# Kernel tuning notes

Measured on AMD Instinct MI355X. Metric: run time of the kernel, lower is better.

Reference implementation:

```python
import jax, jax.numpy as jnp
import numpy as np

EMBED = 1024
HEADS = 16
HEAD_DIM = EMBED // HEADS
SCALE = HEAD_DIM ** -0.5


def setup_inputs() -> dict:
    key = jax.random.key(0)
    ks = jax.random.split(key, 9)
    B, N = 2, 2048
    std = EMBED ** -0.5
    return {
        "query": jax.random.normal(ks[0], (B, N, EMBED), jnp.float32),
        "key": jax.random.normal(ks[1], (B, N, EMBED), jnp.float32),
        "value": jax.random.normal(ks[2], (B, N, EMBED), jnp.float32),
        # torch nn.Linear weights are [out, in]; y = x @ W.T + b
        "Wq": jax.random.normal(ks[3], (EMBED, EMBED), jnp.float32) * std,
        "bq": jax.random.normal(ks[4], (EMBED,), jnp.float32) * 0.01,
        "Wk": jax.random.normal(ks[5], (EMBED, EMBED), jnp.float32) * std,
        "bk": jax.random.normal(ks[6], (EMBED,), jnp.float32) * 0.01,
        "Wv": jax.random.normal(ks[7], (EMBED, EMBED), jnp.float32) * std,
        "bv": jax.random.normal(ks[8], (EMBED,), jnp.float32) * 0.01,
    }


def reference(query, key, value, Wq, bq, Wk, bk, Wv, bv):
    B, NQ, _ = query.shape
    NK = key.shape[1]
    q = query @ Wq.T + bq  # [B, NQ, E]
    k = key @ Wk.T + bk    # [B, NK, E]
    v = value @ Wv.T + bv  # [B, NK, E]
    # split heads -> [B, H, N, Dh]
    q = q.reshape(B, NQ, HEADS, HEAD_DIM).transpose(0, 2, 1, 3)
    k = k.reshape(B, NK, HEADS, HEAD_DIM).transpose(0, 2, 1, 3)
    v = v.reshape(B, NK, HEADS, HEAD_DIM).transpose(0, 2, 1, 3)
    attn = jnp.einsum("bhqd,bhkd->bhqk", q, k) * SCALE  # [B, H, NQ, NK]
    attn = jax.nn.softmax(attn, axis=-1)
    out = jnp.einsum("bhqk,bhkd->bhqd", attn, v)  # [B, H, NQ, Dh]
    out = out.transpose(0, 2, 1, 3).reshape(B, NQ, EMBED)
    # o_proj is Identity (odim == embed_dim, o_proj=False); dropout is 0 (eval)
    return out
```

## Files before the change

### kernel.cpp

```cpp
#include <hip/hip_runtime.h>

#define EMB 1024
#define NSEQ 2048
#define NBATCH 2
#define NHEAD 16
#define DHEAD 64
#define QSCALE 0.18033688011112042f

typedef float f32x4 __attribute__((ext_vector_type(4)));
typedef short s16x8 __attribute__((ext_vector_type(8)));
typedef short s16x4 __attribute__((ext_vector_type(4)));

typedef __attribute__((address_space(3))) short lds_short;
typedef __attribute__((address_space(1))) const short glb_short;

__device__ __forceinline__ void gl_lds16(const short* g, short* l) {
    __builtin_amdgcn_global_load_lds((glb_short*)g, (lds_short*)l, 16, 0, 0);
}

__device__ __forceinline__ short bf16r(float f) {
    unsigned u = __float_as_uint(f);
    u += 0x7fffu + ((u >> 16) & 1u);
    return (short)(u >> 16);
}

__device__ __forceinline__ unsigned pkbf(float a, float b) {
#if defined(__has_builtin) && __has_builtin(__builtin_amdgcn_cvt_pk_bf16_f32)
    auto r = __builtin_amdgcn_cvt_pk_bf16_f32(a, b);
    unsigned u;
    __builtin_memcpy(&u, &r, 4);
    return u;
#else
    return ((unsigned)bf16r(a) & 0xffffu) | ((unsigned)bf16r(b) << 16);
#endif
}

__device__ __forceinline__ float fexp2(float x) {
#if defined(__has_builtin) && __has_builtin(__builtin_amdgcn_exp2f)
    return __builtin_amdgcn_exp2f(x);
#else
    return exp2f(x);
#endif
}

__global__ __launch_bounds__(256) void cvt6_kernel(
    const float* __restrict__ s0, const float* __restrict__ s1, const float* __restrict__ s2,
    const float* __restrict__ s3, const float* __restrict__ s4, const float* __restrict__ s5,
    short* __restrict__ d0, short* __restrict__ d1, short* __restrict__ d2,
    short* __restrict__ d3, short* __restrict__ d4, short* __restrict__ d5,
    int n0, int n1, int n2, int n3, int n4, int n5)
{
    const int seg = blockIdx.y;
    const float* s = (seg == 0) ? s0 : (seg == 1) ? s1 : (seg == 2) ? s2
                   : (seg == 3) ? s3 : (seg == 4) ? s4 : s5;
    short* d = (seg == 0) ? d0 : (seg == 1) ? d1 : (seg == 2) ? d2
             : (seg == 3) ? d3 : (seg == 4) ? d4 : d5;
    const int n = (seg == 0) ? n0 : (seg == 1) ? n1 : (seg == 2) ? n2
                : (seg == 3) ? n3 : (seg == 4) ? n4 : n5;

    const int i = (blockIdx.x * 256 + threadIdx.x) * 8;
    if (i >= n) return;
    float4 a = *(const float4*)(s + i);
    float4 b = *(const float4*)(s + i + 4);
    uint4 u = { pkbf(a.x, a.y), pkbf(a.z, a.w), pkbf(b.x, b.y), pkbf(b.z, b.w) };
    *(uint4*)(d + i) = u;
}

__global__ __launch_bounds__(256, 3) void proj2_kernel(
    const short* __restrict__ Xq, const short* __restrict__ Xk, const short* __restrict__ Xv,
    const short* __restrict__ Wq, const short* __restrict__ Wk, const short* __restrict__ Wv,
    const float* __restrict__ bq, const float* __restrict__ bk, const float* __restrict__ bv,
    short* __restrict__ Oq, short* __restrict__ Ok, short* __restrict__ Ov)
{
    const int z = blockIdx.z;
    const short* X    = (z == 0) ? Xq : (z == 1) ? Xk : Xv;
    const short* W    = (z == 0) ? Wq : (z == 1) ? Wk : Wv;
    const float* bias = (z == 0) ? bq : (z == 1) ? bk : bv;
    short* Out        = (z == 0) ? Oq : (z == 1) ? Ok : Ov;
    const float osc   = (z == 0) ? QSCALE : 1.0f;

    const int n0 = blockIdx.x * 128;
    const int m0 = blockIdx.y * 128;

    __shared__ __align__(16) short As[128 * 64];
    __shared__ __align__(16) short Bs[128 * 64];

    const int t    = threadIdx.x;
    const int lane = t & 63;
    const int wave = t >> 6;
    const int r    = lane & 15;
    const int quad = lane >> 4;
    const int wm   = (wave >> 1) * 64;
    const int wn   = (wave & 1) * 64;

    const int p0    = wave * 256 + lane;
    const int row0  = p0 >> 3;
    const int lc0   = (p0 & 7) ^ (row0 & 7);
    const short* gA = X + (size_t)(m0 + row0) * EMB + lc0 * 8;
    const short* gB = W + (size_t)(n0 + row0) * EMB + lc0 * 8;
    short* lA = As + p0 * 8;
    short* lB = Bs + p0 * 8;

    f32x4 acc[4][4];
#pragma unroll
    for (int i = 0; i < 4; ++i)
#pragma unroll
        for (int j = 0; j < 4; ++j)
#pragma unroll
            for (int v = 0; v < 4; ++v) acc[i][j][v] = 0.f;

    for (int k0 = 0; k0 < EMB; k0 += 64) {
#pragma unroll
        for (int i = 0; i < 4; ++i) {
            gl_lds16(gA + k0 + (size_t)8 * i * EMB, lA + i * 512);
            gl_lds16(gB + k0 + (size_t)8 * i * EMB, lB + i * 512);
        }
        __syncthreads();

#pragma unroll
        for (int ks = 0; ks < 2; ++ks) {
            const int fc = ((ks * 4 + quad) ^ (r & 7)) * 8;
            s16x8 af[4], bf[4];
#pragma unroll
            for (int i = 0; i < 4; ++i) af[i] = *(const s16x8*)&As[(wm + i * 16 + r) * 64 + fc];
#pragma unroll
            for (int j = 0; j < 4; ++j) bf[j] = *(const s16x8*)&Bs[(wn + j * 16 + r) * 64 + fc];
#pragma unroll
            for (int i = 0; i < 4; ++i)
#pragma unroll
                for (int j = 0; j < 4; ++j)
                    acc[i][j] = __builtin_amdgcn_mfma_f32_16x16x32_bf16(af[i], bf[j], acc[i][j], 0, 0, 0);
        }
        __syncthreads();
    }

    if (z != 2) {
#pragma unroll
        for (int j = 0; j < 4; ++j) {
            const int gn = n0 + wn + j * 16 + r;
            const float bb = bias[gn];
#pragma unroll
            for (int i = 0; i < 4; ++i)
#pragma unroll
                for (int reg = 0; reg < 4; ++reg) {
                    const int gm = m0 + wm + i * 16 + quad * 4 + reg;
                    Out[(size_t)gm * EMB + gn] = bf16r((acc[i][j][reg] + bb) * osc);
                }
        }
    } else {
#pragma unroll
        for (int j = 0; j < 4; ++j) {
            const int gn = n0 + wn + j * 16 + r;
            const float bb = bias[gn];
            const int hh = gn >> 6;
            const int dd = gn & 63;
#pragma unroll
            for (int i = 0; i < 4; ++i) {
                const int gm = m0 + wm + i * 16 + quad * 4;
                const int bi = gm >> 11;
                const int nn = gm & 2047;
                s16x4 pk;
#pragma unroll
                for (int reg = 0; reg < 4; ++reg) pk[reg] = bf16r(acc[i][j][reg] + bb);
                *(s16x4*)(Out + ((size_t)(bi * NHEAD + hh) * DHEAD + dd) * NSEQ + nn) = pk;
            }
        }
    }
}

__global__ __launch_bounds__(256) void proj_kernel(
    const float* __restrict__ Xq, const float* __restrict__ Xk, const float* __restrict__ Xv,
    const float* __restrict__ Wq, const float* __restrict__ Wk, const float* __restrict__ Wv,
    const float* __restrict__ bq, const float* __restrict__ bk, const float* __restrict__ bv,
    short* __restrict__ Oq, short* __restrict__ Ok, short* __restrict__ Ov)
{
    const int z = blockIdx.z;
    const float* X    = (z == 0) ? Xq : (z == 1) ? Xk : Xv;
    const float* W    = (z == 0) ? Wq : (z == 1) ? Wk : Wv;
    const float* bias = (z == 0) ? bq : (z == 1) ? bk : bv;
    short* Out        = (z == 0) ? Oq : (z == 1) ? Ok : Ov;
    const float osc   = (z == 0) ? QSCALE : 1.0f;

    const int n0 = blockIdx.x * 128;
    const int m0 = blockIdx.y * 128;

    __shared__ __align__(16) short As[128][40];
    __shared__ __align__(16) short Bs[128][40];

    const int t    = threadIdx.x;
    const int lane = t & 63;
    const int wave = t >> 6;
    const int r    = lane & 15;
    const int quad = lane >> 4;
    const int wm   = (wave >> 1) * 64;
    const int wn   = (wave & 1) * 64;

    const int srow = t >> 1;
    const int scol = (t & 1) << 4;

    f32x4 acc[4][4];
#pragma unroll
    for (int i = 0; i < 4; ++i)
#pragma unroll
        for (int j = 0; j < 4; ++j)
#pragma unroll
            for (int v = 0; v < 4; ++v) acc[i][j][v] = 0.f;

    for (int k0 = 0; k0 < EMB; k0 += 32) {
        const float4* xp = (const float4*)(X + (size_t)(m0 + srow) * EMB + k0 + scol);
        const float4* wp = (const float4*)(W + (size_t)(n0 + srow) * EMB + k0 + scol);
        float4 x0 = xp[0], x1 = xp[1], x2 = xp[2], x3 = xp[3];
        float4 w0 = wp[0], w1 = wp[1], w2 = wp[2], w3 = wp[3];
        uint4 a0 = { pkbf(x0.x, x0.y), pkbf(x0.z, x0.w), pkbf(x1.x, x1.y), pkbf(x1.z, x1.w) };
        uint4 a1 = { pkbf(x2.x, x2.y), pkbf(x2.z, x2.w), pkbf(x3.x, x3.y), pkbf(x3.z, x3.w) };
        uint4 b0 = { pkbf(w0.x, w0.y), pkbf(w0.z, w0.w), pkbf(w1.x, w1.y), pkbf(w1.z, w1.w) };
        uint4 b1 = { pkbf(w2.x, w2.y), pkbf(w2.z, w2.w), pkbf(w3.x, w3.y), pkbf(w3.z, w3.w) };
        *(uint4*)&As[srow][scol]     = a0;
        *(uint4*)&As[srow][scol + 8] = a1;
        *(uint4*)&Bs[srow][scol]     = b0;
        *(uint4*)&Bs[srow][scol + 8] = b1;
        __syncthreads();

        s16x8 af[4], bf[4];
#pragma unroll
        for (int i = 0; i < 4; ++i) af[i] = *(const s16x8*)&As[wm + i * 16 + r][quad * 8];
#pragma unroll
        for (int j = 0; j < 4; ++j) bf[j] = *(const s16x8*)&Bs[wn + j * 16 + r][quad * 8];
#pragma unroll
        for (int i = 0; i < 4; ++i)
#pragma unroll
            for (int j = 0; j < 4; ++j)
                acc[i][j] = __builtin_amdgcn_mfma_f32_16x16x32_bf16(af[i], bf[j], acc[i][j], 0, 0, 0);
        __syncthreads();
    }

#pragma unroll
    for (int j = 0; j < 4; ++j) {
        const int gn = n0 + wn + j * 16 + r;
        const float bb = bias[gn];
#pragma unroll
        for (int i = 0; i < 4; ++i)
#pragma unroll
            for (int reg = 0; reg < 4; ++reg) {
                const int gm = m0 + wm + i * 16 + quad * 4 + reg;
                Out[(size_t)gm * EMB + gn] = bf16r((acc[i][j][reg] + bb) * osc);
            }
    }
}

__global__ __launch_bounds__(256) void vtrans_kernel(
    const short* __restrict__ Vp, short* __restrict__ VT)
{
    const int n0 = blockIdx.x * 64;
    const int h  = blockIdx.y;
    const int b  = blockIdx.z;
    __shared__ __align__(16) short L[64][72];

    const int t  = threadIdx.x;
    const int rr = t >> 2;
    const int cc = (t & 3) * 16;

    const short* src = Vp + (size_t)(b * NSEQ + n0 + rr) * EMB + h * DHEAD + cc;
    s16x8 a = *(const s16x8*)src;
    s16x8 c = *(const s16x8*)(src + 8);
    *(s16x8*)&L[rr][cc]     = a;
    *(s16x8*)&L[rr][cc + 8] = c;
    __syncthreads();

    const int d  = t >> 2;
    const int c4 = (t & 3) * 16;
    short vals[16];
#pragma unroll
    for (int i = 0; i < 16; ++i) vals[i] = L[c4 + i][d];
    short* dst = VT + ((size_t)(b * NHEAD + h) * DHEAD + d) * NSEQ + n0 + c4;
    *(s16x8*)dst       = *(s16x8*)&vals[0];
    *(s16x8*)(dst + 8) = *(s16x8*)&vals[8];
}

template<bool PARTIAL>
__global__ __launch_bounds__(256, 3) void attn11_kernel(
    const short* __restrict__ Qp, const short* __restrict__ Kp,
    const short* __restrict__ VT, float* __restrict__ Outp,
    float* __restrict__ Lout)
{
    const int ksplit = PARTIAL ? (blockIdx.x & 1) : 0;
    const int qblk   = (PARTIAL ? (blockIdx.x >> 1) : blockIdx.x) * 128;
    const int h      = blockIdx.y;
    const int b      = blockIdx.z;
    const int nt     = PARTIAL ? 8 : 16;
    const int kt0    = PARTIAL ? ksplit * 8 : 0;

    __shared__ __align__(16) char smem[32768];
    short* Ks   = (short*)smem;
    short* Vs   = (short*)smem + 128 * 64;
    float* fbuf = (float*)smem;

    const int t    = threadIdx.x;
    const int lane = t & 63;
    const int w    = t >> 6;
    const int r    = lane & 15;
    const int quad = lane >> 4;
    const int r7   = r & 7;

    const size_t rowbase = (size_t)b * NSEQ;
    const int    colbase = h * DHEAD;
    const size_t bh64    = (size_t)(b * NHEAD + h) * DHEAD;

    s16x8 qf[2][2];
#pragma unroll
    for (int qs = 0; qs < 2; ++qs)
#pragma unroll
        for (int ks = 0; ks < 2; ++ks)
            qf[qs][ks] = *(const s16x8*)(Qp + (rowbase + qblk + w * 32 + qs * 16 + r) * EMB
                                          + colbase + ks * 32 + quad * 8);

    f32x4 accO[2][4];
#pragma unroll
    for (int qs = 0; qs < 2; ++qs)
#pragma unroll
        for (int dt = 0; dt < 4; ++dt)
#pragma unroll
            for (int v = 0; v < 4; ++v) accO[qs][dt][v] = 0.f;
    float lsum[2] = {0.f, 0.f};
    const f32x4 zf = {0.f, 0.f, 0.f, 0.f};

    const int  krow0 = t >> 3;
    const int  kgc   = ((t & 7) ^ (krow0 & 7)) * 8;
    const int  vrow0 = t >> 4;
    const int  vgc   = ((t & 15) ^ (vrow0 & 7)) * 8;
    const short* gK[4];
    const short* gV[4];
    {
        const short* kb0 = Kp + (rowbase + kt0 * 128 + krow0) * EMB + colbase + kgc;
        const short* vb0 = VT + (bh64 + vrow0) * NSEQ + kt0 * 128 + vgc;
#pragma unroll
        for (int i = 0; i < 4; ++i) {
            gK[i] = kb0 + (size_t)i * 32 * EMB;
            gV[i] = vb0 + (size_t)i * 16 * NSEQ;
        }
    }
    short* lK[4];
    short* lV[4];
#pragma unroll
    for (int i = 0; i < 4; ++i) {
        lK[i] = Ks + (i * 256 + t) * 8;
        lV[i] = Vs + (i * 256 + t) * 8;
    }

    const int kofs = (quad ^ r7) * 8;
    int vofs[4];
    {
        const int x4  = r7 & 4;
        const int qr3 = ((quad >> 1) ^ r7) & 3;
#pragma unroll
        for (int s = 0; s < 4; ++s)
            vofs[s] = ((((s << 2) ^ x4) | qr3) * 8) + (quad & 1) * 4;
    }

    for (int it = 0; it < nt; ++it) {
#pragma unroll
        for (int i = 0; i < 4; ++i) {
            gl_lds16(gK[i], lK[i]);
            gl_lds16(gV[i], lV[i]);
        }
#pragma unroll
        for (int i = 0; i < 4; ++i) {
            gK[i] += (size_t)128 * EMB;
            gV[i] += 128;
        }
        __syncthreads();

        s16x8 pf[2][4];
#pragma unroll
        for (int s = 0; s < 4; ++s) {
            const short* kb = Ks + (s * 32 + r) * 64;
            const s16x8 kf00 = *(const s16x8*)(kb + kofs);
            const s16x8 kf01 = *(const s16x8*)(kb + (kofs ^ 32));
            const s16x8 kf10 = *(const s16x8*)(kb + 1024 + kofs);
            const s16x8 kf11 = *(const s16x8*)(kb + 1024 + (kofs ^ 32));
#pragma unroll
            for (int qs = 0; qs < 2; ++qs) {
                __builtin_amdgcn_s_setprio(1);
                f32x4 s0 = __builtin_amdgcn_mfma_f32_16x16x32_bf16(
                    kf01, qf[qs][1], __builtin_amdgcn_mfma_f32_16x16x32_bf16(kf00, qf[qs][0], zf, 0, 0, 0), 0, 0, 0);
                f32x4 s1 = __builtin_amdgcn_mfma_f32_16x16x32_bf16(
                    kf11, qf[qs][1], __builtin_amdgcn_mfma_f32_16x16x32_bf16(kf10, qf[qs][0], zf, 0, 0, 0), 0, 0, 0);
                __builtin_amdgcn_s_setprio(0);
                float p0[4], p1[4];
#pragma unroll
                for (int reg = 0; reg < 4; ++reg) {
                    p0[reg] = fexp2(s0[reg]);
                    p1[reg] = fexp2(s1[reg]);
                    lsum[qs] += p0[reg] + p1[reg];
                }
                uint4 uu = { pkbf(p0[0], p0[1]), pkbf(p0[2], p0[3]),
                             pkbf(p1[0], p1[1]), pkbf(p1[2], p1[3]) };
                __builtin_memcpy(&pf[qs][s], &uu, 16);
            }
        }

#pragma unroll
        for (int dt = 0; dt < 4; ++dt) {
            const short* vb = Vs + (dt * 16 + r) * 128;
            s16x8 vfl[4];
#pragma unroll
            for (int s = 0; s < 4; ++s) {
                s16x4 lo = *(const s16x4*)(vb + vofs[s]);
                s16x4 hi = *(const s16x4*)(vb + (vofs[s] ^ 16));
                vfl[s] = __builtin_shufflevector(lo, hi, 0, 1, 2, 3, 4, 5, 6, 7);
            }
            __builtin_amdgcn_s_setprio(1);
#pragma unroll
            for (int qs = 0; qs < 2; ++qs)
#pragma unroll
                for (int s = 0; s < 4; ++s)
                    accO[qs][dt] = __builtin_amdgcn_mfma_f32_16x16x32_bf16(vfl[s], pf[qs][s], accO[qs][dt], 0, 0, 0);
            __builtin_amdgcn_s_setprio(0);
        }
        __syncthreads();
    }

    float rl[2];
#pragma unroll
    for (int qs = 0; qs < 2; ++qs) {
        float s = lsum[qs];
        s += __shfl_xor(s, 16);
        s += __shfl_xor(s, 32);
        rl[qs] = PARTIAL ? 1.f : 1.f / s;
        if (PARTIAL && lane < 16)
            Lout[ksplit * (NBATCH * NHEAD * NSEQ)
                 + (b * NHEAD + h) * NSEQ + qblk + w * 32 + qs * 16 + r] = s;
    }
    float* Obase = PARTIAL
        ? Outp + (size_t)ksplit * ((size_t)NBATCH * NSEQ * EMB)
        : Outp;

#pragma unroll
    for (int qs = 0; qs < 2; ++qs) {
        __syncthreads();
#pragma unroll
        for (int dt = 0; dt < 4; ++dt)
#pragma unroll
            for (int reg = 0; reg < 4; ++reg)
                fbuf[(w * 16 + r) * 68 + dt * 16 + quad * 4 + reg] = accO[qs][dt][reg] * rl[qs];
        __syncthreads();
        const int qi   = t >> 2;
        const int c    = (t & 3) * 16;
        const int wsrc = qi >> 4;
        const int rsrc = qi & 15;
        const float4* fp = (const float4*)&fbuf[(wsrc * 16 + rsrc) * 68 + c];
        float4 o0 = fp[0], o1 = fp[1], o2 = fp[2], o3 = fp[3];
        float* op = Obase + (rowbase + qblk + wsrc * 32 + qs * 16 + rsrc) * EMB + colbase + c;
        ((float4*)op)[0] = o0;
        ((float4*)op)[1] = o1;
        ((float4*)op)[2] = o2;
        ((float4*)op)[3] = o3;
    }
}

__global__ __launch_bounds__(256) void comb_kernel(
    const float* __restrict__ O0, const float* __restrict__ O1,
    const float* __restrict__ L0, const float* __restrict__ L1,
    float* __restrict__ Out)
{
    const size_t i = ((size_t)blockIdx.x * 256 + threadIdx.x) * 4;
    const int b = (int)(i >> 21);
    const int q = (int)((i >> 10) & (NSEQ - 1));
    const int h = (int)((i >> 6) & (NHEAD - 1));
    const int li = (b * NHEAD + h) * NSEQ + q;
    const float rl = 1.f / (L0[li] + L1[li]);
    float4 a = *(const float4*)(O0 + i);
    float4 c = *(const float4*)(O1 + i);
    float4 o = { (a.x + c.x) * rl, (a.y + c.y) * rl, (a.z + c.z) * rl, (a.w + c.w) * rl };
    *(float4*)(Out + i) = o;
}

__global__ __launch_bounds__(256) void attn_fb_kernel(
    const short* __restrict__ Qp, const short* __restrict__ Kp,
    const short* __restrict__ Vp, float* __restrict__ Out)
{
    const int qt = blockIdx.x;
    const int h  = blockIdx.y;
    const int b  = blockIdx.z;

    __shared__ __align__(16) short Ks[64][72];
    __shared__ __align__(16) short VsT[64][72];
    __shared__ __align__(16) short Ps[4][16][72];

    const int t    = threadIdx.x;
    const int lane = t & 63;
    const int w    = t >> 6;
    const int r    = lane & 15;
    const int quad = lane >> 4;

    const size_t rowbase = (size_t)b * NSEQ;
    const int colbase    = h * DHEAD;

    const short* Qr = Qp + (rowbase + qt * 64 + w * 16 + r) * EMB + colbase;
    const s16x8 qf0 = *(const s16x8*)(Qr + quad * 8);
    const s16x8 qf1 = *(const s16x8*)(Qr + 32 + quad * 8);

    float mrow[4], lrow[4];
    f32x4 accO[4];
#pragma unroll
    for (int i = 0; i < 4; ++i) {
        mrow[i] = -INFINITY;
        lrow[i] = 0.f;
#pragma unroll
        for (int v = 0; v < 4; ++v) accO[i][v] = 0.f;
    }

    const int srow = t >> 2;
    const int scol = (t & 3) << 4;

    for (int kt = 0; kt < 32; ++kt) {
        const short* Krow = Kp + (rowbase + kt * 64 + srow) * EMB + colbase + scol;
        const short* Vrow = Vp + (rowbase + kt * 64 + srow) * EMB + colbase + scol;
        s16x8 kv0 = *(const s16x8*)Krow;
        s16x8 kv1 = *(const s16x8*)(Krow + 8);
        s16x8 vv0 = *(const s16x8*)Vrow;
        s16x8 vv1 = *(const s16x8*)(Vrow + 8);
        *(s16x8*)&Ks[srow][scol]     = kv0;
        *(s16x8*)&Ks[srow][scol + 8] = kv1;
#pragma unroll
        for (int i = 0; i < 8; ++i) {
            VsT[scol + i][srow]     = vv0[i];
            VsT[scol + 8 + i][srow] = vv1[i];
        }
        __syncthreads();

        f32x4 sacc[4];
#pragma unroll
        for (int j = 0; j < 4; ++j) {
#pragma unroll
            for (int v = 0; v < 4; ++v) sacc[j][v] = 0.f;
            s16x8 kf0 = *(const s16x8*)&Ks[j * 16 + r][quad * 8];
            s16x8 kf1 = *(const s16x8*)&Ks[j * 16 + r][32 + quad * 8];
            sacc[j] = __builtin_amdgcn_mfma_f32_16x16x32_bf16(qf0, kf0, sacc[j], 0, 0, 0);
            sacc[j] = __builtin_amdgcn_mfma_f32_16x16x32_bf16(qf1, kf1, sacc[j], 0, 0, 0);
        }

        float rmax[4];
#pragma unroll
        for (int reg = 0; reg < 4; ++reg) rmax[reg] = -INFINITY;
#pragma unroll
        for (int j = 0; j < 4; ++j)
#pragma unroll
            for (int reg = 0; reg < 4; ++reg)
                rmax[reg] = fmaxf(rmax[reg], sacc[j][reg]);
#pragma unroll
        for (int reg = 0; reg < 4; ++reg) {
#pragma unroll
            for (int mask = 1; mask <= 8; mask <<= 1)
                rmax[reg] = fmaxf(rmax[reg], __shfl_xor(rmax[reg], mask, 64));
        }

        float alpha[4], rsum[4];
#pragma unroll
        for (int reg = 0; reg < 4; ++reg) {
            float mnew = fmaxf(mrow[reg], rmax[reg]);
            alpha[reg] = fexp2(mrow[reg] - mnew);
            mrow[reg]  = mnew;
            rsum[reg]  = 0.f;
        }

#pragma unroll
        for (int j = 0; j < 4; ++j)
#pragma unroll
            for (int reg = 0; reg < 4; ++reg) {
                float p = fexp2(sacc[j][reg] - mrow[reg]);
                rsum[reg] += p;
                Ps[w][quad * 4 + reg][j * 16 + r] = bf16r(p);
            }
#pragma unroll
        for (int reg = 0; reg < 4; ++reg) {
#pragma unroll
            for (int mask = 1; mask <= 8; mask <<= 1)
                rsum[reg] += __shfl_xor(rsum[reg], mask, 64);
            lrow[reg] = lrow[reg] * alpha[reg] + rsum[reg];
        }
#pragma unroll
        for (int j = 0; j < 4; ++j)
#pragma unroll
            for (int reg = 0; reg < 4; ++reg) accO[j][reg] *= alpha[reg];

#pragma unroll
        for (int s = 0; s < 2; ++s) {
            s16x8 pfr = *(const s16x8*)&Ps[w][r][s * 32 + quad * 8];
#pragma unroll
            for (int j = 0; j < 4; ++j) {
                s16x8 vfr = *(const s16x8*)&VsT[j * 16 + r][s * 32 + quad * 8];
                accO[j] = __builtin_amdgcn_mfma_f32_16x16x32_bf16(pfr, vfr, accO[j], 0, 0, 0);
            }
        }
        __syncthreads();
    }

#pragma unroll
    for (int j = 0; j < 4; ++j)
#pragma unroll
        for (int reg = 0; reg < 4; ++reg) {
            const int qrow = qt * 64 + w * 16 + quad * 4 + reg;
            Out[(rowbase + qrow) * EMB + colbase + j * 16 + r] = accO[j][reg] / lrow[reg];
        }
}

extern "C" void kernel_launch(void* const* d_in, const int* in_sizes, int n_in,
                              void* d_out, int out_size, void* d_ws, size_t ws_size,
                              hipStream_t stream) {
    const float* query = (const float*)d_in[0];
    const float* key   = (const float*)d_in[1];
    const float* value = (const float*)d_in[2];
    const float* Wq    = (const float*)d_in[3];
    const float* bq    = (const float*)d_in[4];
    const float* Wk    = (const float*)d_in[5];
    const float* bk    = (const float*)d_in[6];
    const float* Wv    = (const float*)d_in[7];
    const float* bv    = (const float*)d_in[8];
    float* out = (float*)d_out;

    const size_t XBUF = (size_t)NBATCH * NSEQ * EMB;
    const size_t WBUF = (size_t)EMB * EMB;
    const size_t LBUF = (size_t)NBATCH * NHEAD * NSEQ;

    short* Qb  = (short*)d_ws;
    short* Kb  = Qb + XBUF;
    short* Vb  = Kb + XBUF;
    short* VTb = Vb + XBUF;
    short* Xqb = VTb + XBUF;
    short* Xkb = Xqb + XBUF;
    short* Xvb = Xkb + XBUF;
    short* Wqb = Xvb + XBUF;
    short* Wkb = Wqb + WBUF;
    short* Wvb = Wkb + WBUF;
    float* OP  = (float*)(Wvb + WBUF);
    float* LP  = OP + 2 * XBUF;

    const size_t need_full  = (7 * XBUF + 3 * WBUF) * sizeof(short);
    const size_t need_split = need_full + (2 * XBUF + 2 * LBUF) * sizeof(float);
    const size_t need_attn  = 4 * XBUF * sizeof(short);

    if (ws_size >= need_split) {
        cvt6_kernel<<<dim3(2048, 6), 256, 0, stream>>>(
            query, key, value, Wq, Wk, Wv,
            Xqb, Xkb, Xvb, Wqb, Wkb, Wvb,
            (int)XBUF, (int)XBUF, (int)XBUF, (int)WBUF, (int)WBUF, (int)WBUF);
        proj2_kernel<<<dim3(EMB / 128, (NBATCH * NSEQ) / 128, 3), 256, 0, stream>>>(
            Xqb, Xkb, Xvb, Wqb, Wkb, Wvb, bq, bk, bv, Qb, Kb, VTb);
        attn11_kernel<true><<<dim3(2 * NSEQ / 128, NHEAD, NBATCH), 256, 0, stream>>>(
            Qb, Kb, VTb, OP, LP);
        comb_kernel<<<dim3((unsigned)(XBUF / 1024)), 256, 0, stream>>>(
            OP, OP + XBUF, LP, LP + LBUF, out);
    } else if (ws_size >= need_full) {
        cvt6_kernel<<<dim3(2048, 6), 256, 0, stream>>>(
            query, key, value, Wq, Wk, Wv,
            Xqb, Xkb, Xvb, Wqb, Wkb, Wvb,
            (int)XBUF, (int)XBUF, (int)XBUF, (int)WBUF, (int)WBUF, (int)WBUF);
        proj2_kernel<<<dim3(EMB / 128, (NBATCH * NSEQ) / 128, 3), 256, 0, stream>>>(
            Xqb, Xkb, Xvb, Wqb, Wkb, Wvb, bq, bk, bv, Qb, Kb, VTb);
        attn11_kernel<false><<<dim3(NSEQ / 128, NHEAD, NBATCH), 256, 0, stream>>>(
            Qb, Kb, VTb, out, nullptr);
    } else if (ws_size >= need_attn) {
        proj_kernel<<<dim3(EMB / 128, (NBATCH * NSEQ) / 128, 3), 256, 0, stream>>>(
            query, key, value, Wq, Wk, Wv, bq, bk, bv, Qb, Kb, Vb);
        vtrans_kernel<<<dim3(NSEQ / 64, NHEAD, NBATCH), 256, 0, stream>>>(Vb, VTb);
        attn11_kernel<false><<<dim3(NSEQ / 128, NHEAD, NBATCH), 256, 0, stream>>>(
            Qb, Kb, VTb, out, nullptr);
    } else {
        proj_kernel<<<dim3(EMB / 128, (NBATCH * NSEQ) / 128, 3), 256, 0, stream>>>(
            query, key, value, Wq, Wk, Wv, bq, bk, bv, Qb, Kb, Vb);
        attn_fb_kernel<<<dim3(NSEQ / 64, NHEAD, NBATCH), 256, 0, stream>>>(Qb, Kb, Vb, out);
    }
}
```

Baseline: 210.9 us.

## Replace split-KV attention and combine pass with double-buffered single-pass kernel

The attention kernel no longer splits the key range in two. It stops writing fp32 partial outputs and row sums, and the separate combine kernel is removed. It now processes all 16 key tiles in one block, with a 64KB LDS double buffer: the next K/V tile is issued through global_load_lds while the current tile is computed. This removes the partial-output round trip through global memory and one kernel launch. In exchange, occupancy drops (launch bounds 2 and twice the shared memory) and the grid halves to 512 blocks, giving less parallelism to hide latency.

```diff
diff --git a/kernel.cpp b/kernel.cpp
--- a/kernel.cpp
+++ b/kernel.cpp
@@ -277,22 +277,16 @@
     *(s16x8*)(dst + 8) = *(s16x8*)&vals[8];
 }
 
-template<bool PARTIAL>
-__global__ __launch_bounds__(256, 3) void attn11_kernel(
+__global__ __launch_bounds__(256, 2) void attn12_kernel(
     const short* __restrict__ Qp, const short* __restrict__ Kp,
-    const short* __restrict__ VT, float* __restrict__ Outp,
-    float* __restrict__ Lout)
+    const short* __restrict__ VT, float* __restrict__ Out)
 {
-    const int ksplit = PARTIAL ? (blockIdx.x & 1) : 0;
-    const int qblk   = (PARTIAL ? (blockIdx.x >> 1) : blockIdx.x) * 128;
-    const int h      = blockIdx.y;
-    const int b      = blockIdx.z;
-    const int nt     = PARTIAL ? 8 : 16;
-    const int kt0    = PARTIAL ? ksplit * 8 : 0;
-
-    __shared__ __align__(16) char smem[32768];
-    short* Ks   = (short*)smem;
-    short* Vs   = (short*)smem + 128 * 64;
+    const int qblk = blockIdx.x * 128;
+    const int h    = blockIdx.y;
+    const int b    = blockIdx.z;
+
+    __shared__ __align__(16) char smem[65536];
+    short* S    = (short*)smem;
     float* fbuf = (float*)smem;
 
     const int t    = threadIdx.x;
@@ -324,28 +318,25 @@
     float lsum[2] = {0.f, 0.f};
     const f32x4 zf = {0.f, 0.f, 0.f, 0.f};
 
-    const int  krow0 = t >> 3;
-    const int  kgc   = ((t & 7) ^ (krow0 & 7)) * 8;
-    const int  vrow0 = t >> 4;
-    const int  vgc   = ((t & 15) ^ (vrow0 & 7)) * 8;
-    const short* gK[4];
-    const short* gV[4];
+    const int krow0 = t >> 3;
+    const int kgc   = ((t & 7) ^ (krow0 & 7)) * 8;
+    const int vrow0 = t >> 4;
+    const int vgc   = ((t & 15) ^ (vrow0 & 7)) * 8;
+    const short* gKp = Kp + (rowbase + krow0) * EMB + colbase + kgc;
+    const short* gVp = VT + (bh64 + vrow0) * NSEQ + vgc;
+
     {
-        const short* kb0 = Kp + (rowbase + kt0 * 128 + krow0) * EMB + colbase + kgc;
-        const short* vb0 = VT + (bh64 + vrow0) * NSEQ + kt0 * 128 + vgc;
+        short* SK = S;
+        short* SV = S + 8192;
 #pragma unroll
         for (int i = 0; i < 4; ++i) {
-            gK[i] = kb0 + (size_t)i * 32 * EMB;
-            gV[i] = vb0 + (size_t)i * 16 * NSEQ;
-        }
-    }
-    short* lK[4];
-    short* lV[4];
-#pragma unroll
-    for (int i = 0; i < 4; ++i) {
-        lK[i] = Ks + (i * 256 + t) * 8;
-        lV[i] = Vs + (i * 256 + t) * 8;
-    }
+            gl_lds16(gKp + (size_t)i * 32 * EMB, SK + (i * 256 + t) * 8);
+            gl_lds16(gVp + (size_t)i * 16 * NSEQ, SV + (i * 256 + t) * 8);
+        }
+        gKp += (size_t)128 * EMB;
+        gVp += 128;
+    }
+    __syncthreads();
 
     const int kofs = (quad ^ r7) * 8;
     int vofs[4];
@@ -357,18 +348,24 @@
             vofs[s] = ((((s << 2) ^ x4) | qr3) * 8) + (quad & 1) * 4;
     }
 
-    for (int it = 0; it < nt; ++it) {
-#pragma unroll
-        for (int i = 0; i < 4; ++i) {
-            gl_lds16(gK[i], lK[i]);
-            gl_lds16(gV[i], lV[i]);
-        }
-#pragma unroll
-        for (int i = 0; i < 4; ++i) {
-            gK[i] += (size_t)128 * EMB;
-            gV[i] += 128;
-        }
-        __syncthreads();
+#pragma unroll 2
+    for (int it = 0; it < 16; ++it) {
+        const int cur = it & 1;
+
+        if (it + 1 < 16) {
+            short* SKn = S + (cur ^ 1) * 16384;
+            short* SVn = SKn + 8192;
+#pragma unroll
+            for (int i = 0; i < 4; ++i) {
+                gl_lds16(gKp + (size_t)i * 32 * EMB, SKn + (i * 256 + t) * 8);
+                gl_lds16(gVp + (size_t)i * 16 * NSEQ, SVn + (i * 256 + t) * 8);
+            }
+            gKp += (size_t)128 * EMB;
+            gVp += 128;
+        }
+
+        const short* Ks = S + cur * 16384;
+        const short* Vs = Ks + 8192;
 
         s16x8 pf[2][4];
 #pragma unroll
@@ -417,6 +414,7 @@
                     accO[qs][dt] = __builtin_amdgcn_mfma_f32_16x16x32_bf16(vfl[s], pf[qs][s], accO[qs][dt], 0, 0, 0);
             __builtin_amdgcn_s_setprio(0);
         }
+
         __syncthreads();
     }
 
@@ -426,14 +424,8 @@
         float s = lsum[qs];
         s += __shfl_xor(s, 16);
         s += __shfl_xor(s, 32);
-        rl[qs] = PARTIAL ? 1.f : 1.f / s;
-        if (PARTIAL && lane < 16)
-            Lout[ksplit * (NBATCH * NHEAD * NSEQ)
-                 + (b * NHEAD + h) * NSEQ + qblk + w * 32 + qs * 16 + r] = s;
-    }
-    float* Obase = PARTIAL
-        ? Outp + (size_t)ksplit * ((size_t)NBATCH * NSEQ * EMB)
-        : Outp;
+        rl[qs] = 1.f / s;
+    }
 
 #pragma unroll
     for (int qs = 0; qs < 2; ++qs) {
@@ -450,29 +442,12 @@
         const int rsrc = qi & 15;
         const float4* fp = (const float4*)&fbuf[(wsrc * 16 + rsrc) * 68 + c];
         float4 o0 = fp[0], o1 = fp[1], o2 = fp[2], o3 = fp[3];
-        float* op = Obase + (rowbase + qblk + wsrc * 32 + qs * 16 + rsrc) * EMB + colbase + c;
+        float* op = Out + (rowbase + qblk + wsrc * 32 + qs * 16 + rsrc) * EMB + colbase + c;
         ((float4*)op)[0] = o0;
         ((float4*)op)[1] = o1;
         ((float4*)op)[2] = o2;
         ((float4*)op)[3] = o3;
     }
-}
-
-__global__ __launch_bounds__(256) void comb_kernel(
-    const float* __restrict__ O0, const float* __restrict__ O1,
-    const float* __restrict__ L0, const float* __restrict__ L1,
-    float* __restrict__ Out)
-{
-    const size_t i = ((size_t)blockIdx.x * 256 + threadIdx.x) * 4;
-    const int b = (int)(i >> 21);
-    const int q = (int)((i >> 10) & (NSEQ - 1));
-    const int h = (int)((i >> 6) & (NHEAD - 1));
-    const int li = (b * NHEAD + h) * NSEQ + q;
-    const float rl = 1.f / (L0[li] + L1[li]);
-    float4 a = *(const float4*)(O0 + i);
-    float4 c = *(const float4*)(O1 + i);
-    float4 o = { (a.x + c.x) * rl, (a.y + c.y) * rl, (a.z + c.z) * rl, (a.w + c.w) * rl };
-    *(float4*)(Out + i) = o;
 }
 
 __global__ __launch_bounds__(256) void attn_fb_kernel(
@@ -621,7 +596,6 @@
 
     const size_t XBUF = (size_t)NBATCH * NSEQ * EMB;
     const size_t WBUF = (size_t)EMB * EMB;
-    const size_t LBUF = (size_t)NBATCH * NHEAD * NSEQ;
 
     short* Qb  = (short*)d_ws;
     short* Kb  = Qb + XBUF;
@@ -633,39 +607,25 @@
     short* Wqb = Xvb + XBUF;
     short* Wkb = Wqb + WBUF;
     short* Wvb = Wkb + WBUF;
-    float* OP  = (float*)(Wvb + WBUF);
-    float* LP  = OP + 2 * XBUF;
-
-    const size_t need_full  = (7 * XBUF + 3 * WBUF) * sizeof(short);
-    const size_t need_split = need_full + (2 * XBUF + 2 * LBUF) * sizeof(float);
-    const size_t need_attn  = 4 * XBUF * sizeof(short);
-
-    if (ws_size >= need_split) {
+
+    const size_t need_full = (7 * XBUF + 3 * WBUF) * sizeof(short);
+    const size_t need_attn = 4 * XBUF * sizeof(short);
+
+    if (ws_size >= need_full) {
         cvt6_kernel<<<dim3(2048, 6), 256, 0, stream>>>(
             query, key, value, Wq, Wk, Wv,
             Xqb, Xkb, Xvb, Wqb, Wkb, Wvb,
             (int)XBUF, (int)XBUF, (int)XBUF, (int)WBUF, (int)WBUF, (int)WBUF);
         proj2_kernel<<<dim3(EMB / 128, (NBATCH * NSEQ) / 128, 3), 256, 0, stream>>>(
             Xqb, Xkb, Xvb, Wqb, Wkb, Wvb, bq, bk, bv, Qb, Kb, VTb);
-        attn11_kernel<true><<<dim3(2 * NSEQ / 128, NHEAD, NBATCH), 256, 0, stream>>>(
-            Qb, Kb, VTb, OP, LP);
-        comb_kernel<<<dim3((unsigned)(XBUF / 1024)), 256, 0, stream>>>(
-            OP, OP + XBUF, LP, LP + LBUF, out);
-    } else if (ws_size >= need_full) {
-        cvt6_kernel<<<dim3(2048, 6), 256, 0, stream>>>(
-            query, key, value, Wq, Wk, Wv,
-            Xqb, Xkb, Xvb, Wqb, Wkb, Wvb,
-            (int)XBUF, (int)XBUF, (int)XBUF, (int)WBUF, (int)WBUF, (int)WBUF);
-        proj2_kernel<<<dim3(EMB / 128, (NBATCH * NSEQ) / 128, 3), 256, 0, stream>>>(
-            Xqb, Xkb, Xvb, Wqb, Wkb, Wvb, bq, bk, bv, Qb, Kb, VTb);
-        attn11_kernel<false><<<dim3(NSEQ / 128, NHEAD, NBATCH), 256, 0, stream>>>(
-            Qb, Kb, VTb, out, nullptr);
+        attn12_kernel<<<dim3(NSEQ / 128, NHEAD, NBATCH), 256, 0, stream>>>(
+            Qb, Kb, VTb, out);
     } else if (ws_size >= need_attn) {
         proj_kernel<<<dim3(EMB / 128, (NBATCH * NSEQ) / 128, 3), 256, 0, stream>>>(
             query, key, value, Wq, Wk, Wv, bq, bk, bv, Qb, Kb, Vb);
         vtrans_kernel<<<dim3(NSEQ / 64, NHEAD, NBATCH), 256, 0, stream>>>(Vb, VTb);
-        attn11_kernel<false><<<dim3(NSEQ / 128, NHEAD, NBATCH), 256, 0, stream>>>(
-            Qb, Kb, VTb, out, nullptr);
+        attn12_kernel<<<dim3(NSEQ / 128, NHEAD, NBATCH), 256, 0, stream>>>(
+            Qb, Kb, VTb, out);
     } else {
         proj_kernel<<<dim3(EMB / 128, (NBATCH * NSEQ) / 128, 3), 256, 0, stream>>>(
             query, key, value, Wq, Wk, Wv, bq, bk, bv, Qb, Kb, Vb);
```

Result: faster. 199.6 us (-5.4%).
